# Performance work log

Hardware: AMD Instinct MI355X
Metric: run time of the kernel (lower is better)

## Reference

```python
import jax, jax.numpy as jnp
import numpy as np

EPS = 1e-5

def _bn(x, g, b):
    # BatchNorm3d in training mode over (batch, spatial) dims; x: [B, C, N]
    mean = jnp.mean(x, axis=(0, 2), keepdims=True)
    var = jnp.var(x, axis=(0, 2), keepdims=True)
    return g[None, :, None] * (x - mean) * jax.lax.rsqrt(var + EPS) + b[None, :, None]


def setup_inputs() -> dict:
    key = jax.random.key(0)
    ks = jax.random.split(key, 6)
    B, C, N, K, H = 2, 128, 32768, 9, 512
    x = jax.random.normal(ks[0], (B, C, N, 1), dtype=jnp.float32)
    edge_index = jax.random.randint(ks[1], (2, B, N, K), 0, N, dtype=jnp.int32)
    s = 0.05
    return {
        "x": x,
        "edge_index": edge_index,
        "w_mr": jax.random.normal(ks[2], (C, 2 * C), dtype=jnp.float32) * s,
        "b_mr": jnp.zeros((C,), jnp.float32),
        "g_mr": jnp.ones((C,), jnp.float32),
        "be_mr": jnp.zeros((C,), jnp.float32),
        "w1": jax.random.normal(ks[3], (H, C), dtype=jnp.float32) * s,
        "b1": jnp.zeros((H,), jnp.float32),
        "g1": jnp.ones((H,), jnp.float32),
        "be1": jnp.zeros((H,), jnp.float32),
        "w2": jax.random.normal(ks[4], (C, H), dtype=jnp.float32) * s,
        "b2": jnp.zeros((C,), jnp.float32),
        "g2": jnp.ones((C,), jnp.float32),
        "be2": jnp.zeros((C,), jnp.float32),
    }


def reference(x, edge_index, w_mr, b_mr, g_mr, be_mr, w1, b1, g1, be1, w2, b2, g2, be2):
    # x: [B, C, N, 1], edge_index: [2, B, N, K]
    B, C, N, _ = x.shape
    x2 = x[..., 0]  # [B, C, N]

    # batched_index_select: gather node features along N for each (B, N, K) index
    gather = jax.vmap(lambda xb, ib: xb[:, ib])  # ([C,N],[N,K]) -> [C,N,K]
    x_i = gather(x2, edge_index[1])  # [B, C, N, K] center features
    x_j = gather(x2, edge_index[0])  # [B, C, N, K] neighbor features
    rel = jnp.max(x_j - x_i, axis=-1)  # max-relative reduction -> [B, C, N]

    # torch.cat([x.unsqueeze(2), rel.unsqueeze(2)], 2).reshape(B, 2C, N): interleaved channels
    feat = jnp.stack([x2, rel], axis=2).reshape(B, 2 * C, N)

    # BasicConv([2C, C]): Conv3d 1x1 -> BN -> ReLU
    y = jnp.einsum('oc,bcn->bon', w_mr, feat) + b_mr[None, :, None]
    y = jax.nn.relu(_bn(y, g_mr, be_mr))

    # FFN: conv1x1 C->H, BN, ReLU, conv1x1 H->C, BN, residual
    h = jnp.einsum('hc,bcn->bhn', w1, y) + b1[None, :, None]
    h = jax.nn.relu(_bn(h, g1, be1))
    out = jnp.einsum('ch,bhn->bcn', w2, h) + b2[None, :, None]
    out = _bn(out, g2, be2) + y
    return out  # [B, C, N]
```

## Files before the change

### kernel.cpp

```cpp
#include <hip/hip_runtime.h>
#include <hip/hip_bf16.h>
#include <cstddef>
#include <cstdint>

#define BB 2
#define CC 128
#define NN 32768
#define KNBR 9
#define HH 512
#define PP (BB * NN)
#define TWO_C 256
#define EPSBN 1e-5f

typedef __attribute__((ext_vector_type(4))) float f32x4;
typedef __attribute__((ext_vector_type(8))) short s16x8;
typedef __attribute__((ext_vector_type(4))) unsigned int u32x4;

__device__ __forceinline__ float bf2f(unsigned int u) {
    return __uint_as_float(u << 16);
}
__device__ __forceinline__ unsigned short f2bf(float f) {
    unsigned int u = __float_as_uint(f);
    u += 0x7fffu + ((u >> 16) & 1u);
    return (unsigned short)(u >> 16);
}

__global__ __launch_bounds__(256) void transpose_kernel(
    const float* __restrict__ x, unsigned short* __restrict__ xT) {
    __shared__ float t[32][129];
    const int b = blockIdx.y;
    const int n0 = blockIdx.x * 32;
    const int tid = threadIdx.x;
    {
        const int tn = tid % 32;
        const int cq = tid / 32;
        for (int c = cq; c < CC; c += 8)
            t[tn][c] = x[((size_t)b * CC + c) * NN + n0 + tn];
    }
    __syncthreads();
    {
        const int ct = tid % 128;
        const int nq = tid / 128;
        for (int nl = nq; nl < 32; nl += 2)
            xT[((size_t)b * NN + n0 + nl) * CC + ct] = f2bf(t[nl][ct]);
    }
}

__global__ __launch_bounds__(256) void gather_kernel(
    const unsigned short* __restrict__ xT, const int* __restrict__ ei,
    unsigned short* __restrict__ featT) {
    const int pt = blockIdx.x * 4 + (threadIdx.x >> 6);
    const int lane = threadIdx.x & 63;
    const int b = pt >> 15;
    const int n = pt & (NN - 1);
    const unsigned short* xb = xT + (size_t)b * NN * CC;
    const int* e0 = ei + ((size_t)b * NN + n) * KNBR;
    const int* e1 = ei + ((size_t)(BB + b) * NN + n) * KNBR;

    const unsigned int xv = *(const unsigned int*)(xb + (size_t)n * CC + lane * 2);
    float m0 = -INFINITY, m1 = -INFINITY;
#pragma unroll
    for (int k = 0; k < KNBR; k++) {
        const int j0 = e0[k], j1 = e1[k];
        const unsigned int va = *(const unsigned int*)(xb + (size_t)j0 * CC + lane * 2);
        const unsigned int vb = *(const unsigned int*)(xb + (size_t)j1 * CC + lane * 2);
        m0 = fmaxf(m0, bf2f(va & 0xffffu) - bf2f(vb & 0xffffu));
        m1 = fmaxf(m1, bf2f(va >> 16) - bf2f(vb >> 16));
    }
    ushort4 o;
    o.x = (unsigned short)(xv & 0xffffu);
    o.y = f2bf(m0);
    o.z = (unsigned short)(xv >> 16);
    o.w = f2bf(m1);
    *(ushort4*)(featT + (size_t)pt * TWO_C + lane * 4) = o;
}

__global__ __launch_bounds__(256) void wconv_kernel(
    const float* __restrict__ w_mr, const float* __restrict__ w1,
    const float* __restrict__ w2, unsigned short* __restrict__ o_mr,
    unsigned short* __restrict__ o1, unsigned short* __restrict__ o2) {
    const int i = blockIdx.x * 256 + threadIdx.x;
    if (i < CC * TWO_C) o_mr[i] = f2bf(w_mr[i]);
    o1[i] = f2bf(w1[i]);
    o2[i] = f2bf(w2[i]);
}

template <int KTOT, int OC, bool ACT>
__global__ __launch_bounds__(256) void mgemm_kernel(
    const unsigned short* __restrict__ A,
    const unsigned short* __restrict__ W,
    const float* __restrict__ bias,
    const float* __restrict__ act,
    unsigned short* __restrict__ Cout,
    float* __restrict__ stats) {
    __shared__ __align__(16) unsigned short As[128 * 64];
    __shared__ __align__(16) unsigned short Bs[128 * 64];
    __shared__ float bsA[256];
    __shared__ float bsB[256];

    const int tid = threadIdx.x;
    const int pb = blockIdx.x * 128;
    const int ob = blockIdx.y * 128;
    const int w = tid >> 6;
    const int wr = w >> 1, wc = w & 1;
    const int lane = tid & 63;
    const int lm = lane & 15, lg = lane >> 4;

    f32x4 acc[4][4] = {};

    for (int k0 = 0; k0 < KTOT; k0 += 64) {
#pragma unroll
        for (int i = 0; i < 4; i++) {
            const int idx = tid + i * 256;
            const int row = idx >> 3;
            const int kb = (idx & 7) * 16;
            const int sw = kb ^ ((row & 7) << 4);
            {
                const char* src = (const char*)(A + (size_t)(pb + row) * KTOT + k0) + kb;
                if (!ACT) {
                    const u32x4 v = *(const u32x4*)src;
                    *(u32x4*)((char*)As + row * 128 + sw) = v;
                } else {
                    const s16x8 v = *(const s16x8*)src;
                    const int ke = k0 + (kb >> 1);
                    const f32x4 sa0 = *(const f32x4*)(act + ke);
                    const f32x4 sa1 = *(const f32x4*)(act + ke + 4);
                    const f32x4 sb0 = *(const f32x4*)(act + KTOT + ke);
                    const f32x4 sb1 = *(const f32x4*)(act + KTOT + ke + 4);
                    s16x8 r;
#pragma unroll
                    for (int j = 0; j < 4; j++) {
                        const float f = bf2f((unsigned short)v[j]);
                        r[j] = (short)f2bf(fmaxf(fmaf(sa0[j], f, sb0[j]), 0.f));
                    }
#pragma unroll
                    for (int j = 0; j < 4; j++) {
                        const float f = bf2f((unsigned short)v[4 + j]);
                        r[4 + j] = (short)f2bf(fmaxf(fmaf(sa1[j], f, sb1[j]), 0.f));
                    }
                    *(s16x8*)((char*)As + row * 128 + sw) = r;
                }
            }
            {
                const char* src = (const char*)(W + (size_t)(ob + row) * KTOT + k0) + kb;
                const u32x4 v = *(const u32x4*)src;
                *(u32x4*)((char*)Bs + row * 128 + sw) = v;
            }
        }
        __syncthreads();
#pragma unroll
        for (int kk = 0; kk < 2; kk++) {
            s16x8 aF[4], bF[4];
            const int kbyte = kk * 64 + lg * 16;
#pragma unroll
            for (int m = 0; m < 4; m++) {
                const int r = wr * 64 + m * 16 + lm;
                aF[m] = *(const s16x8*)((const char*)As + r * 128 + (kbyte ^ ((r & 7) << 4)));
            }
#pragma unroll
            for (int n = 0; n < 4; n++) {
                const int c = wc * 64 + n * 16 + lm;
                bF[n] = *(const s16x8*)((const char*)Bs + c * 128 + (kbyte ^ ((c & 7) << 4)));
            }
#pragma unroll
            for (int m = 0; m < 4; m++)
#pragma unroll
                for (int n = 0; n < 4; n++)
                    acc[m][n] = __builtin_amdgcn_mfma_f32_16x16x32_bf16(
                        aF[m], bF[n], acc[m][n], 0, 0, 0);
        }
        __syncthreads();
    }

    float sA[4] = {0.f, 0.f, 0.f, 0.f};
    float sB[4] = {0.f, 0.f, 0.f, 0.f};
#pragma unroll
    for (int n = 0; n < 4; n++) {
        const int o = ob + wc * 64 + n * 16 + lm;
        const float bo = bias[o];
#pragma unroll
        for (int m = 0; m < 4; m++) {
            const size_t p = (size_t)pb + wr * 64 + m * 16 + lg * 4;
#pragma unroll
            for (int j = 0; j < 4; j++) {
                const float h = acc[m][n][j] + bo;
                Cout[(p + j) * OC + o] = f2bf(h);
                sA[n] += h;
                sB[n] = fmaf(h, h, sB[n]);
            }
        }
    }
#pragma unroll
    for (int n = 0; n < 4; n++) {
        float a = sA[n], q = sB[n];
        a += __shfl_xor(a, 16); a += __shfl_xor(a, 32);
        q += __shfl_xor(q, 16); q += __shfl_xor(q, 32);
        if (lg == 0) {
            bsA[wr * 128 + wc * 64 + n * 16 + lm] = a;
            bsB[wr * 128 + wc * 64 + n * 16 + lm] = q;
        }
    }
    __syncthreads();
    if (tid < 128) {
        atomicAdd(&stats[ob + tid], bsA[tid] + bsA[128 + tid]);
        atomicAdd(&stats[OC + ob + tid], bsB[tid] + bsB[128 + tid]);
    }
}

__global__ void finalize_kernel(const float* __restrict__ stats,
                                const float* __restrict__ g,
                                const float* __restrict__ be,
                                float* __restrict__ act, int CH, float invP) {
    const int c = blockIdx.x * blockDim.x + threadIdx.x;
    if (c < CH) {
        const float mean = stats[c] * invP;
        const float var = stats[CH + c] * invP - mean * mean;
        const float a = g[c] * rsqrtf(var + EPSBN);
        act[c] = a;
        act[CH + c] = be[c] - mean * a;
    }
}

__global__ __launch_bounds__(256) void final_kernel(
    const unsigned short* __restrict__ y_bf, const unsigned short* __restrict__ o_bf,
    const float* __restrict__ act1, const float* __restrict__ act3,
    float* __restrict__ out) {
    __shared__ float t[32][129];
    const int b = blockIdx.y;
    const int n0 = blockIdx.x * 32;
    const int tid = threadIdx.x;
    {
        const int lane = tid & 63;
        const int rq = tid >> 6;
        const int c0 = lane * 2;
        const float a1x = act1[c0], a1y = act1[c0 + 1];
        const float b1x = act1[CC + c0], b1y = act1[CC + c0 + 1];
        const float a3x = act3[c0], a3y = act3[c0 + 1];
        const float b3x = act3[CC + c0], b3y = act3[CC + c0 + 1];
        for (int rl = rq; rl < 32; rl += 4) {
            const size_t p = (size_t)b * NN + n0 + rl;
            const unsigned int yv = *(const unsigned int*)(y_bf + p * CC + c0);
            const unsigned int ov = *(const unsigned int*)(o_bf + p * CC + c0);
            t[rl][c0]     = fmaf(a3x, bf2f(ov & 0xffffu), b3x) +
                            fmaxf(fmaf(a1x, bf2f(yv & 0xffffu), b1x), 0.f);
            t[rl][c0 + 1] = fmaf(a3y, bf2f(ov >> 16), b3y) +
                            fmaxf(fmaf(a1y, bf2f(yv >> 16), b1y), 0.f);
        }
    }
    __syncthreads();
    {
        const int tn = tid % 32;
        const int cq = tid / 32;
        for (int c = cq; c < CC; c += 8)
            out[((size_t)b * CC + c) * NN + n0 + tn] = t[tn][c];
    }
}

extern "C" void kernel_launch(void* const* d_in, const int* in_sizes, int n_in,
                              void* d_out, int out_size, void* d_ws, size_t ws_size,
                              hipStream_t stream) {
    const float* x     = (const float*)d_in[0];
    const int*   ei    = (const int*)d_in[1];
    const float* w_mr  = (const float*)d_in[2];
    const float* b_mr  = (const float*)d_in[3];
    const float* g_mr  = (const float*)d_in[4];
    const float* be_mr = (const float*)d_in[5];
    const float* w1    = (const float*)d_in[6];
    const float* b1    = (const float*)d_in[7];
    const float* g1    = (const float*)d_in[8];
    const float* be1   = (const float*)d_in[9];
    const float* w2    = (const float*)d_in[10];
    const float* b2    = (const float*)d_in[11];
    const float* g2    = (const float*)d_in[12];
    const float* be2   = (const float*)d_in[13];
    float* out = (float*)d_out;

    char* ws = (char*)d_ws;
    unsigned short* xT    = (unsigned short*)(ws + 0);
    unsigned short* featT = (unsigned short*)(ws + 16777216);
    unsigned short* y_bf  = (unsigned short*)(ws + 50331648);
    unsigned short* h_bf  = (unsigned short*)(ws + 67108864);
    unsigned short* o_bf  = (unsigned short*)(ws + 134217728);
    unsigned short* wmr_b = (unsigned short*)(ws + 150994944);
    unsigned short* w1_b  = (unsigned short*)(ws + 151060480);
    unsigned short* w2_b  = (unsigned short*)(ws + 151191552);
    float* stats1 = (float*)(ws + 151322624);
    float* stats2 = (float*)(ws + 151323648);
    float* stats3 = (float*)(ws + 151327744);
    float* act1   = (float*)(ws + 151328768);
    float* act2   = (float*)(ws + 151329792);
    float* act3   = (float*)(ws + 151333888);

    const float invP = 1.0f / (float)PP;

    hipMemsetAsync(stats1, 0, 6144, stream);

    transpose_kernel<<<dim3(NN / 32, BB), 256, 0, stream>>>(x, xT);
    gather_kernel<<<PP / 4, 256, 0, stream>>>(xT, ei, featT);
    wconv_kernel<<<256, 256, 0, stream>>>(w_mr, w1, w2, wmr_b, w1_b, w2_b);

    mgemm_kernel<TWO_C, CC, false><<<dim3(PP / 128, 1), 256, 0, stream>>>(
        featT, wmr_b, b_mr, act1, y_bf, stats1);
    finalize_kernel<<<1, CC, 0, stream>>>(stats1, g_mr, be_mr, act1, CC, invP);

    mgemm_kernel<CC, HH, true><<<dim3(PP / 128, HH / 128), 256, 0, stream>>>(
        y_bf, w1_b, b1, act1, h_bf, stats2);
    finalize_kernel<<<1, HH, 0, stream>>>(stats2, g1, be1, act2, HH, invP);

    mgemm_kernel<HH, CC, true><<<dim3(PP / 128, 1), 256, 0, stream>>>(
        h_bf, w2_b, b2, act2, o_bf, stats3);
    finalize_kernel<<<1, CC, 0, stream>>>(stats3, g2, be2, act3, CC, invP);

    final_kernel<<<dim3(NN / 32, BB), 256, 0, stream>>>(y_bf, o_bf, act1, act3, out);
}
```

Baseline: 171.1 us.

## Load GEMM MFMA fragments directly from global memory, dropping LDS staging

The bf16 MFMA GEMM kernels no longer stage A and W tiles through swizzled shared memory with barriers. Each wave now loads its 16x8 fragments straight from global memory per 32-wide K step and applies the fused BN+ReLU on the fly. This removes LDS traffic and __syncthreads. In exchange, the two column-warps of a block each load the A rows separately, and the loads are strided per lane, relying on L1/L2 for reuse and coalescing.

```diff
diff --git a/kernel.cpp b/kernel.cpp
--- a/kernel.cpp
+++ b/kernel.cpp
@@ -14,7 +14,6 @@
 
 typedef __attribute__((ext_vector_type(4))) float f32x4;
 typedef __attribute__((ext_vector_type(8))) short s16x8;
-typedef __attribute__((ext_vector_type(4))) unsigned int u32x4;
 
 __device__ __forceinline__ float bf2f(unsigned int u) {
     return __uint_as_float(u << 16);
@@ -86,15 +85,13 @@
 }
 
 template <int KTOT, int OC, bool ACT>
-__global__ __launch_bounds__(256) void mgemm_kernel(
+__global__ __launch_bounds__(256) void dgemm_kernel(
     const unsigned short* __restrict__ A,
     const unsigned short* __restrict__ W,
     const float* __restrict__ bias,
     const float* __restrict__ act,
     unsigned short* __restrict__ Cout,
     float* __restrict__ stats) {
-    __shared__ __align__(16) unsigned short As[128 * 64];
-    __shared__ __align__(16) unsigned short Bs[128 * 64];
     __shared__ float bsA[256];
     __shared__ float bsB[256];
 
@@ -106,70 +103,47 @@
     const int lane = tid & 63;
     const int lm = lane & 15, lg = lane >> 4;
 
+    const unsigned short* Ab = A + (size_t)(pb + wr * 64 + lm) * KTOT + lg * 8;
+    const unsigned short* Wb = W + (size_t)(ob + wc * 64 + lm) * KTOT + lg * 8;
+
     f32x4 acc[4][4] = {};
 
-    for (int k0 = 0; k0 < KTOT; k0 += 64) {
-#pragma unroll
-        for (int i = 0; i < 4; i++) {
-            const int idx = tid + i * 256;
-            const int row = idx >> 3;
-            const int kb = (idx & 7) * 16;
-            const int sw = kb ^ ((row & 7) << 4);
-            {
-                const char* src = (const char*)(A + (size_t)(pb + row) * KTOT + k0) + kb;
-                if (!ACT) {
-                    const u32x4 v = *(const u32x4*)src;
-                    *(u32x4*)((char*)As + row * 128 + sw) = v;
-                } else {
-                    const s16x8 v = *(const s16x8*)src;
-                    const int ke = k0 + (kb >> 1);
-                    const f32x4 sa0 = *(const f32x4*)(act + ke);
-                    const f32x4 sa1 = *(const f32x4*)(act + ke + 4);
-                    const f32x4 sb0 = *(const f32x4*)(act + KTOT + ke);
-                    const f32x4 sb1 = *(const f32x4*)(act + KTOT + ke + 4);
-                    s16x8 r;
-#pragma unroll
-                    for (int j = 0; j < 4; j++) {
-                        const float f = bf2f((unsigned short)v[j]);
-                        r[j] = (short)f2bf(fmaxf(fmaf(sa0[j], f, sb0[j]), 0.f));
-                    }
-#pragma unroll
-                    for (int j = 0; j < 4; j++) {
-                        const float f = bf2f((unsigned short)v[4 + j]);
-                        r[4 + j] = (short)f2bf(fmaxf(fmaf(sa1[j], f, sb1[j]), 0.f));
-                    }
-                    *(s16x8*)((char*)As + row * 128 + sw) = r;
-                }
+    for (int k0 = 0; k0 < KTOT; k0 += 32) {
+        s16x8 aF[4], bF[4];
+        f32x4 sa0, sa1, sb0, sb1;
+        if (ACT) {
+            const int ke = k0 + lg * 8;
+            sa0 = *(const f32x4*)(act + ke);
+            sa1 = *(const f32x4*)(act + ke + 4);
+            sb0 = *(const f32x4*)(act + KTOT + ke);
+            sb1 = *(const f32x4*)(act + KTOT + ke + 4);
+        }
+#pragma unroll
+        for (int n = 0; n < 4; n++)
+            bF[n] = *(const s16x8*)(Wb + (size_t)n * 16 * KTOT + k0);
+#pragma unroll
+        for (int m = 0; m < 4; m++) {
+            s16x8 v = *(const s16x8*)(Ab + (size_t)m * 16 * KTOT + k0);
+            if (ACT) {
+                s16x8 r;
+#pragma unroll
+                for (int j = 0; j < 4; j++)
+                    r[j] = (short)f2bf(
+                        fmaxf(fmaf(sa0[j], bf2f((unsigned short)v[j]), sb0[j]), 0.f));
+#pragma unroll
+                for (int j = 0; j < 4; j++)
+                    r[4 + j] = (short)f2bf(
+                        fmaxf(fmaf(sa1[j], bf2f((unsigned short)v[4 + j]), sb1[j]), 0.f));
+                v = r;
             }
-            {
-                const char* src = (const char*)(W + (size_t)(ob + row) * KTOT + k0) + kb;
-                const u32x4 v = *(const u32x4*)src;
-                *(u32x4*)((char*)Bs + row * 128 + sw) = v;
-            }
-        }
-        __syncthreads();
-#pragma unroll
-        for (int kk = 0; kk < 2; kk++) {
-            s16x8 aF[4], bF[4];
-            const int kbyte = kk * 64 + lg * 16;
-#pragma unroll
-            for (int m = 0; m < 4; m++) {
-                const int r = wr * 64 + m * 16 + lm;
-                aF[m] = *(const s16x8*)((const char*)As + r * 128 + (kbyte ^ ((r & 7) << 4)));
-            }
-#pragma unroll
-            for (int n = 0; n < 4; n++) {
-                const int c = wc * 64 + n * 16 + lm;
-                bF[n] = *(const s16x8*)((const char*)Bs + c * 128 + (kbyte ^ ((c & 7) << 4)));
-            }
-#pragma unroll
-            for (int m = 0; m < 4; m++)
-#pragma unroll
-                for (int n = 0; n < 4; n++)
-                    acc[m][n] = __builtin_amdgcn_mfma_f32_16x16x32_bf16(
-                        aF[m], bF[n], acc[m][n], 0, 0, 0);
-        }
-        __syncthreads();
+            aF[m] = v;
+        }
+#pragma unroll
+        for (int m = 0; m < 4; m++)
+#pragma unroll
+            for (int n = 0; n < 4; n++)
+                acc[m][n] = __builtin_amdgcn_mfma_f32_16x16x32_bf16(
+                    aF[m], bF[n], acc[m][n], 0, 0, 0);
     }
 
     float sA[4] = {0.f, 0.f, 0.f, 0.f};
@@ -299,15 +273,15 @@
     gather_kernel<<<PP / 4, 256, 0, stream>>>(xT, ei, featT);
     wconv_kernel<<<256, 256, 0, stream>>>(w_mr, w1, w2, wmr_b, w1_b, w2_b);
 
-    mgemm_kernel<TWO_C, CC, false><<<dim3(PP / 128, 1), 256, 0, stream>>>(
+    dgemm_kernel<TWO_C, CC, false><<<dim3(PP / 128, 1), 256, 0, stream>>>(
         featT, wmr_b, b_mr, act1, y_bf, stats1);
     finalize_kernel<<<1, CC, 0, stream>>>(stats1, g_mr, be_mr, act1, CC, invP);
 
-    mgemm_kernel<CC, HH, true><<<dim3(PP / 128, HH / 128), 256, 0, stream>>>(
+    dgemm_kernel<CC, HH, true><<<dim3(PP / 128, HH / 128), 256, 0, stream>>>(
         y_bf, w1_b, b1, act1, h_bf, stats2);
     finalize_kernel<<<1, HH, 0, stream>>>(stats2, g1, be1, act2, HH, invP);
 
-    mgemm_kernel<HH, CC, true><<<dim3(PP / 128, 1), 256, 0, stream>>>(
+    dgemm_kernel<HH, CC, true><<<dim3(PP / 128, 1), 256, 0, stream>>>(
         h_bf, w2_b, b2, act2, o_bf, stats3);
     finalize_kernel<<<1, CC, 0, stream>>>(stats3, g2, be2, act3, CC, invP);
 
```

New measurement: 215.4 us. 1.26x slower.
